# Performance work log

Measured on AMD Instinct MI355X. Metric: run time of the kernel, lower is better.

The kernel has to match this reference:

```python
import jax, jax.numpy as jnp
import numpy as np

BETA = 0.25

def _l2norm(x, eps=1e-12):
    # F.normalize(x, dim=-1)
    n = jnp.sqrt(jnp.sum(x * x, axis=-1, keepdims=True))
    return x / jnp.maximum(n, eps)

def setup_inputs() -> dict:
    key = jax.random.key(0)
    k1, k2 = jax.random.split(key)
    z = jax.random.normal(k1, (32, 1024, 32), dtype=jnp.float32)
    embedding = jax.random.normal(k2, (8192, 32), dtype=jnp.float32)
    return {"z": z, "embedding": embedding}

def reference(z, embedding):
    B, T, D = z.shape
    zf = _l2norm(z.reshape(-1, D))            # [N, D]
    en = _l2norm(embedding)                   # [n_e, D]
    # squared distances: ||z||^2 + ||e||^2 - 2 z.e  -> [N, n_e]
    d = (jnp.sum(zf * zf, axis=1, keepdims=True)
         + jnp.sum(en * en, axis=1)
         - 2.0 * jnp.einsum('nd,kd->nk', zf, en))
    idx = jnp.argmin(d, axis=1).reshape(B, T)            # [B, T]
    z_q = embedding[idx]                                  # [B, T, D] gather
    z_qnorm = _l2norm(z_q)
    z_norm = _l2norm(z)
    loss = (BETA * jnp.mean((jax.lax.stop_gradient(z_qnorm) - z_norm) ** 2)
            + jnp.mean((z_qnorm - jax.lax.stop_gradient(z_norm)) ** 2))
    # straight-through estimator
    z_q_out = z + jax.lax.stop_gradient(z_qnorm - z)
    return z_q_out, loss, idx
```

## Files before the change

### kernel.cpp

```cpp
#include <hip/hip_runtime.h>
#include <math.h>


#define D 32
#define KCODES 8192
#define MARGIN 2.5e-4f
#define EPS 1e-12f

typedef short bf16x8 __attribute__((ext_vector_type(8)));
typedef unsigned short u16x8 __attribute__((ext_vector_type(8)));
typedef float f32x4 __attribute__((ext_vector_type(4)));

static __device__ __forceinline__ unsigned short f2bf(float x) {
  unsigned u = __float_as_uint(x);
  return (unsigned short)((u + 0x7FFFu + ((u >> 16) & 1u)) >> 16);
}
static __device__ __forceinline__ float bf2f(unsigned short s) {
  return __uint_as_float(((unsigned)s) << 16);
}
static __device__ __forceinline__ void gload_lds16(const void* g, void* l) {
  __builtin_amdgcn_global_load_lds(
      (const __attribute__((address_space(1))) void*)g,
      (__attribute__((address_space(3))) void*)l, 16, 0, 0);
}


__global__ __launch_bounds__(256) void k_prep(const float* __restrict__ z,
                                              const float* __restrict__ emb,
                                              float* __restrict__ en,
                                              float* __restrict__ en_h,
                                              unsigned short* __restrict__ eswz,
                                              unsigned short* __restrict__ zswz_hi,
                                              unsigned short* __restrict__ zswz_lo,
                                              int* __restrict__ cnt,
                                              float* __restrict__ loss,
                                              unsigned long long* __restrict__ mp2,
                                              int N) {
  int v = blockIdx.x * 256 + threadIdx.x;
  if (v == 0) { *cnt = 0; *loss = 0.f; }
  if (v >= KCODES + N) return;
  if (v >= KCODES) mp2[v - KCODES] = 0ull;
  const float* src = (v < KCODES) ? (emb + (size_t)v * D) : (z + (size_t)(v - KCODES) * D);

  float x[D];
  const float4* p = reinterpret_cast<const float4*>(src);
#pragma unroll
  for (int j = 0; j < D / 4; ++j) {
    float4 q = p[j];
    x[4 * j + 0] = q.x; x[4 * j + 1] = q.y; x[4 * j + 2] = q.z; x[4 * j + 3] = q.w;
  }
  float ss = 0.f;
#pragma unroll
  for (int j = 0; j < D; ++j) ss = fmaf(x[j], x[j], ss);
  float n = fmaxf(sqrtf(ss), EPS);
#pragma unroll
  for (int j = 0; j < D; ++j) x[j] = x[j] / n;

  unsigned short hi[D], lo[D];
#pragma unroll
  for (int j = 0; j < D; ++j) {
    hi[j] = f2bf(x[j]);
    lo[j] = f2bf(x[j] - bf2f(hi[j]));
  }

  if (v < KCODES) {
    float4* o = reinterpret_cast<float4*>(en + (size_t)v * D);
    float s2 = 0.f;
#pragma unroll
    for (int j = 0; j < D / 4; ++j) {
      float4 q = {x[4 * j], x[4 * j + 1], x[4 * j + 2], x[4 * j + 3]};
      s2 = fmaf(q.x, q.x, fmaf(q.y, q.y, fmaf(q.z, q.z, fmaf(q.w, q.w, s2))));
      o[j] = q;
    }
    en_h[v] = 0.5f * s2;
    int tl = v >> 4, m = v & 15;
#pragma unroll
    for (int q = 0; q < 4; ++q) {
      u16x8 hv, lv;
#pragma unroll
      for (int j = 0; j < 8; ++j) { hv[j] = hi[8 * q + j]; lv[j] = lo[8 * q + j]; }
      *(u16x8*)(eswz + (size_t)tl * 1024 + (q * 16 + m) * 8) = hv;
      *(u16x8*)(eswz + (size_t)tl * 1024 + 512 + (q * 16 + m) * 8) = lv;
    }
  } else {
    int r = v - KCODES;
    int g = r >> 4, m = r & 15;
#pragma unroll
    for (int q = 0; q < 4; ++q) {
      u16x8 hv, lv;
#pragma unroll
      for (int j = 0; j < 8; ++j) { hv[j] = hi[8 * q + j]; lv[j] = lo[8 * q + j]; }
      *(u16x8*)(zswz_hi + (size_t)g * 512 + (q * 16 + m) * 8) = hv;
      *(u16x8*)(zswz_lo + (size_t)g * 512 + (q * 16 + m) * 8) = lv;
    }
  }
}

__global__ __launch_bounds__(256, 2) void k_argmin_mfma(
    const unsigned short* __restrict__ zswz_hi,
    const unsigned short* __restrict__ zswz_lo,
    const unsigned short* __restrict__ eswz,
    int* __restrict__ idx_ws, int* __restrict__ list, int* __restrict__ cnt) {
  __shared__ unsigned short lds_sh[2][16384];

  const int tid = threadIdx.x;
  const int wid = tid >> 6, lane = tid & 63;
  const int lane15 = lane & 15, quad = lane >> 4;
  const int g = blockIdx.x * 4 + wid;

  const bf16x8 zhi = *(const bf16x8*)(zswz_hi + (size_t)g * 512 + lane * 8);
  const bf16x8 zlo = *(const bf16x8*)(zswz_lo + (size_t)g * 512 + lane * 8);

  float s1[4], s2[4];
  int kb[4];
#pragma unroll
  for (int r = 0; r < 4; ++r) { s1[r] = -3.4e38f; s2[r] = -3.4e38f; kb[r] = 0; }
  const f32x4 zero4 = {0.f, 0.f, 0.f, 0.f};

  const float4* gall = reinterpret_cast<const float4*>(eswz);
#pragma unroll
  for (int i = 0; i < 8; ++i) {
    int off = i * 256 + tid;
    gload_lds16(gall + off, (char*)&lds_sh[0][0] + (size_t)off * 16);
  }

  for (int c = 0; c < 32; ++c) {
    __syncthreads();
    if (c + 1 < 32) {
      const float4* gn = gall + (size_t)(c + 1) * 2048;
      char* dst = (char*)&lds_sh[(c + 1) & 1][0];
#pragma unroll
      for (int i = 0; i < 8; ++i) {
        int off = i * 256 + tid;
        gload_lds16(gn + off, dst + (size_t)off * 16);
      }
    }
    const unsigned short* buf = &lds_sh[c & 1][0];
    int kcur = c * 256 + lane15;
#pragma unroll
    for (int t = 0; t < 16; ++t) {
      bf16x8 bhi = *(const bf16x8*)(buf + t * 1024 + lane * 8);
      bf16x8 blo = *(const bf16x8*)(buf + t * 1024 + 512 + lane * 8);
      f32x4 acc = __builtin_amdgcn_mfma_f32_16x16x32_bf16(zhi, bhi, zero4, 0, 0, 0);
      acc = __builtin_amdgcn_mfma_f32_16x16x32_bf16(zhi, blo, acc, 0, 0, 0);
      acc = __builtin_amdgcn_mfma_f32_16x16x32_bf16(zlo, bhi, acc, 0, 0, 0);
#pragma unroll
      for (int r = 0; r < 4; ++r) {
        float cv = acc[r];
        bool cond = cv > s1[r];
        kb[r] = cond ? kcur : kb[r];
        s2[r] = fmaxf(s2[r], fminf(cv, s1[r]));
        s1[r] = fmaxf(s1[r], cv);
      }
      kcur += 16;
    }
  }

  unsigned long long packed[4];
#pragma unroll
  for (int r = 0; r < 4; ++r) {
    unsigned o = __float_as_uint(s1[r]);
    o = (o & 0x80000000u) ? ~o : (o | 0x80000000u);
    packed[r] = ((unsigned long long)o << 32) | (unsigned)(8191 - kb[r]);
  }
#pragma unroll
  for (int m = 1; m <= 8; m <<= 1) {
#pragma unroll
    for (int r = 0; r < 4; ++r) {
      unsigned long long op = __shfl_xor(packed[r], m, 64);
      float os1 = __shfl_xor(s1[r], m, 64);
      float os2 = __shfl_xor(s2[r], m, 64);
      s2[r] = fmaxf(fmaxf(s2[r], os2), fminf(s1[r], os1));
      s1[r] = fmaxf(s1[r], os1);
      packed[r] = (op > packed[r]) ? op : packed[r];
    }
  }
  if (lane15 == 0) {
#pragma unroll
    for (int r = 0; r < 4; ++r) {
      int row = g * 16 + quad * 4 + r;
      if (s1[r] - s2[r] < MARGIN) {
        int pos = atomicAdd(cnt, 1);
        list[pos] = row;
        idx_ws[row] = -(pos + 1);
      } else {
        idx_ws[row] = 8191 - (int)(unsigned)(packed[r] & 0xFFFFFFFFull);
      }
    }
  }
}

__global__ __launch_bounds__(256) void k_cleanup(const float* __restrict__ z,
                                                 const float* __restrict__ en,
                                                 const float* __restrict__ en_h,
                                                 const int* __restrict__ list,
                                                 const int* __restrict__ cnt,
                                                 unsigned long long* __restrict__ mp2) {
  __shared__ unsigned long long wred[4];
  const int tid = threadIdx.x;
  const int lane = tid & 63, wid = tid >> 6;
  const int ntask = (*cnt) * 32;

  for (int j = blockIdx.x; j < ntask; j += gridDim.x) {
    int i = j >> 5, kc = j & 31;
    int row = list[i];
    const float* zr = z + (size_t)row * D;
    float v[D];
    float ss = 0.f;
#pragma unroll
    for (int d = 0; d < D; ++d) v[d] = zr[d];
#pragma unroll
    for (int d = 0; d < D; ++d) ss = fmaf(v[d], v[d], ss);
    float n = fmaxf(sqrtf(ss), EPS);
#pragma unroll
    for (int d = 0; d < D; ++d) v[d] = v[d] / n;

    int k = kc * 256 + tid;
    const float4* er = reinterpret_cast<const float4*>(en + (size_t)k * D);
    float a = -en_h[k];
#pragma unroll
    for (int jj = 0; jj < 8; ++jj) {
      float4 e = er[jj];
      a = fmaf(v[4 * jj + 0], e.x, a);
      a = fmaf(v[4 * jj + 1], e.y, a);
      a = fmaf(v[4 * jj + 2], e.z, a);
      a = fmaf(v[4 * jj + 3], e.w, a);
    }
    unsigned o = __float_as_uint(a);
    o = (o & 0x80000000u) ? ~o : (o | 0x80000000u);
    unsigned long long pk = ((unsigned long long)o << 32) | (unsigned)(8191 - k);
#pragma unroll
    for (int m = 32; m >= 1; m >>= 1) {
      unsigned long long op = __shfl_xor(pk, m, 64);
      pk = (op > pk) ? op : pk;
    }
    if (lane == 0) wred[wid] = pk;
    __syncthreads();
    if (tid == 0) {
      unsigned long long m01 = (wred[0] > wred[1]) ? wred[0] : wred[1];
      unsigned long long m23 = (wred[2] > wred[3]) ? wred[2] : wred[3];
      atomicMax(&mp2[i], (m01 > m23) ? m01 : m23);
    }
    __syncthreads();
  }
}

__global__ __launch_bounds__(256) void k_epi(const float* __restrict__ z,
                                             const float* __restrict__ en,
                                             const int* __restrict__ idx_ws,
                                             const unsigned long long* __restrict__ mp2,
                                             float* __restrict__ out_z,
                                             float* __restrict__ loss,
                                             float* __restrict__ out_idx,
                                             float scale) {
  int row = blockIdx.x * 256 + threadIdx.x;
  int kb = idx_ws[row];
  if (kb < 0) {
    unsigned long long m = mp2[-kb - 1];
    kb = 8191 - (int)(unsigned)(m & 0xFFFFFFFFull);
  }
  out_idx[row] = (float)kb;

  const float4* p = reinterpret_cast<const float4*>(z + (size_t)row * D);
  float4 q[D / 4];
#pragma unroll
  for (int j = 0; j < D / 4; ++j) q[j] = p[j];
  float ss = 0.f;
#pragma unroll
  for (int j = 0; j < D / 4; ++j)
    ss = fmaf(q[j].x, q[j].x, fmaf(q[j].y, q[j].y, fmaf(q[j].z, q[j].z, fmaf(q[j].w, q[j].w, ss))));
  float n = fmaxf(sqrtf(ss), EPS);

  const float4* ep = reinterpret_cast<const float4*>(en + (size_t)kb * D);
  float4* op = reinterpret_cast<float4*>(out_z + (size_t)row * D);
  float s = 0.f;
#pragma unroll
  for (int j = 0; j < D / 4; ++j) {
    float4 e = ep[j];
    float4 o;
    o.x = q[j].x + (e.x - q[j].x);
    o.y = q[j].y + (e.y - q[j].y);
    o.z = q[j].z + (e.z - q[j].z);
    o.w = q[j].w + (e.w - q[j].w);
    op[j] = o;
    float dx = e.x - q[j].x / n;  float dy = e.y - q[j].y / n;
    float dz = e.z - q[j].z / n;  float dw = e.w - q[j].w / n;
    s = fmaf(dx, dx, fmaf(dy, dy, fmaf(dz, dz, fmaf(dw, dw, s))));
  }

#pragma unroll
  for (int off = 32; off > 0; off >>= 1) s += __shfl_down(s, off, 64);
  __shared__ float wsum[4];
  int lane = threadIdx.x & 63, wid = threadIdx.x >> 6;
  if (lane == 0) wsum[wid] = s;
  __syncthreads();
  if (threadIdx.x == 0) {
    float tt = (wsum[0] + wsum[1]) + (wsum[2] + wsum[3]);
    atomicAdd(loss, tt * scale);
  }
}

extern "C" void kernel_launch(void* const* d_in, const int* in_sizes, int n_in,
                              void* d_out, int out_size, void* d_ws, size_t ws_size,
                              hipStream_t stream) {
  const float* z = (const float*)d_in[0];
  const float* emb = (const float*)d_in[1];
  const int N = in_sizes[0] / D;
  const int K = in_sizes[1] / D;

  float* out = (float*)d_out;
  float* out_z = out;
  float* loss = out + (size_t)N * D;
  float* out_idx = out + (size_t)N * D + 1;

  char* w = (char*)d_ws;
  float* en = (float*)w;                         w += (size_t)K * D * 4;
  float* en_h = (float*)w;                       w += (size_t)K * 4;
  unsigned short* eswz = (unsigned short*)w;     w += (size_t)K * D * 2 * 2;
  unsigned short* zswz_hi = (unsigned short*)w;  w += (size_t)N * D * 2;
  unsigned short* zswz_lo = (unsigned short*)w;  w += (size_t)N * D * 2;
  int* idx_ws = (int*)w;                         w += (size_t)N * 4;
  int* list = (int*)w;                           w += (size_t)N * 4;
  unsigned long long* mp2 = (unsigned long long*)w; w += (size_t)N * 8;
  int* cnt = (int*)w;

  k_prep<<<dim3((K + N) / 256), 256, 0, stream>>>(
      z, emb, en, en_h, eswz, zswz_hi, zswz_lo, cnt, loss, mp2, N);

  k_argmin_mfma<<<dim3(N / 64), 256, 0, stream>>>(
      zswz_hi, zswz_lo, eswz, idx_ws, list, cnt);

  k_cleanup<<<dim3(4096), 256, 0, stream>>>(z, en, en_h, list, cnt, mp2);

  k_epi<<<dim3(N / 256), 256, 0, stream>>>(
      z, en, idx_ws, mp2, out_z, loss, out_idx, 1.25f / (float)((size_t)N * D));
}
```

Baseline: 188.3 us.

## Fuse z normalization into argmin kernel and pack score with index

Moves the per-row z normalization and bf16 hi/lo split out of the prep kernel and into the argmin kernel, so the z staging buffers and their global round-trip go away. The top-2 tracking now packs a truncated positive score with a 9-bit tile index into one unsigned word, which makes the inner compare cheaper. The score is kept positive by seeding the accumulator with a constant offset. LDS B-fragment loads are software-prefetched one step ahead. The packing loses low mantissa bits, so the near-tie margin is widened, which may send more rows to the cleanup pass. The cleanup grid is halved and mp2 is now zeroed per list entry.

```diff
diff --git a/kernel.cpp b/kernel.cpp
--- a/kernel.cpp
+++ b/kernel.cpp
@@ -4,7 +4,7 @@
 
 #define D 32
 #define KCODES 8192
-#define MARGIN 2.5e-4f
+#define MARGIN_Q 5.0e-4f
 #define EPS 1e-12f
 
 typedef short bf16x8 __attribute__((ext_vector_type(8)));
@@ -25,25 +25,18 @@
 }
 
 
-__global__ __launch_bounds__(256) void k_prep(const float* __restrict__ z,
-                                              const float* __restrict__ emb,
+__global__ __launch_bounds__(256) void k_prep(const float* __restrict__ emb,
                                               float* __restrict__ en,
                                               float* __restrict__ en_h,
                                               unsigned short* __restrict__ eswz,
-                                              unsigned short* __restrict__ zswz_hi,
-                                              unsigned short* __restrict__ zswz_lo,
                                               int* __restrict__ cnt,
-                                              float* __restrict__ loss,
-                                              unsigned long long* __restrict__ mp2,
-                                              int N) {
+                                              float* __restrict__ loss) {
   int v = blockIdx.x * 256 + threadIdx.x;
   if (v == 0) { *cnt = 0; *loss = 0.f; }
-  if (v >= KCODES + N) return;
-  if (v >= KCODES) mp2[v - KCODES] = 0ull;
-  const float* src = (v < KCODES) ? (emb + (size_t)v * D) : (z + (size_t)(v - KCODES) * D);
+  if (v >= KCODES) return;
 
   float x[D];
-  const float4* p = reinterpret_cast<const float4*>(src);
+  const float4* p = reinterpret_cast<const float4*>(emb + (size_t)v * D);
 #pragma unroll
   for (int j = 0; j < D / 4; ++j) {
     float4 q = p[j];
@@ -56,51 +49,38 @@
 #pragma unroll
   for (int j = 0; j < D; ++j) x[j] = x[j] / n;
 
+  float4* o = reinterpret_cast<float4*>(en + (size_t)v * D);
+  float s2 = 0.f;
+#pragma unroll
+  for (int j = 0; j < D / 4; ++j) {
+    float4 q = {x[4 * j], x[4 * j + 1], x[4 * j + 2], x[4 * j + 3]};
+    s2 = fmaf(q.x, q.x, fmaf(q.y, q.y, fmaf(q.z, q.z, fmaf(q.w, q.w, s2))));
+    o[j] = q;
+  }
+  en_h[v] = 0.5f * s2;
+
   unsigned short hi[D], lo[D];
 #pragma unroll
   for (int j = 0; j < D; ++j) {
     hi[j] = f2bf(x[j]);
     lo[j] = f2bf(x[j] - bf2f(hi[j]));
   }
-
-  if (v < KCODES) {
-    float4* o = reinterpret_cast<float4*>(en + (size_t)v * D);
-    float s2 = 0.f;
-#pragma unroll
-    for (int j = 0; j < D / 4; ++j) {
-      float4 q = {x[4 * j], x[4 * j + 1], x[4 * j + 2], x[4 * j + 3]};
-      s2 = fmaf(q.x, q.x, fmaf(q.y, q.y, fmaf(q.z, q.z, fmaf(q.w, q.w, s2))));
-      o[j] = q;
-    }
-    en_h[v] = 0.5f * s2;
-    int tl = v >> 4, m = v & 15;
-#pragma unroll
-    for (int q = 0; q < 4; ++q) {
-      u16x8 hv, lv;
-#pragma unroll
-      for (int j = 0; j < 8; ++j) { hv[j] = hi[8 * q + j]; lv[j] = lo[8 * q + j]; }
-      *(u16x8*)(eswz + (size_t)tl * 1024 + (q * 16 + m) * 8) = hv;
-      *(u16x8*)(eswz + (size_t)tl * 1024 + 512 + (q * 16 + m) * 8) = lv;
-    }
-  } else {
-    int r = v - KCODES;
-    int g = r >> 4, m = r & 15;
-#pragma unroll
-    for (int q = 0; q < 4; ++q) {
-      u16x8 hv, lv;
-#pragma unroll
-      for (int j = 0; j < 8; ++j) { hv[j] = hi[8 * q + j]; lv[j] = lo[8 * q + j]; }
-      *(u16x8*)(zswz_hi + (size_t)g * 512 + (q * 16 + m) * 8) = hv;
-      *(u16x8*)(zswz_lo + (size_t)g * 512 + (q * 16 + m) * 8) = lv;
-    }
+  int tl = v >> 4, m = v & 15;
+#pragma unroll
+  for (int q = 0; q < 4; ++q) {
+    u16x8 hv, lv;
+#pragma unroll
+    for (int j = 0; j < 8; ++j) { hv[j] = hi[8 * q + j]; lv[j] = lo[8 * q + j]; }
+    *(u16x8*)(eswz + (size_t)tl * 1024 + (q * 16 + m) * 8) = hv;
+    *(u16x8*)(eswz + (size_t)tl * 1024 + 512 + (q * 16 + m) * 8) = lv;
   }
 }
 
 __global__ __launch_bounds__(256, 2) void k_argmin_mfma(
-    const unsigned short* __restrict__ zswz_hi,
-    const unsigned short* __restrict__ zswz_lo,
+    const float* __restrict__ z,
     const unsigned short* __restrict__ eswz,
-    int* __restrict__ idx_ws, int* __restrict__ list, int* __restrict__ cnt) {
+    int* __restrict__ idx_ws, int* __restrict__ list, int* __restrict__ cnt,
+    unsigned long long* __restrict__ mp2) {
   __shared__ unsigned short lds_sh[2][16384];
 
   const int tid = threadIdx.x;
@@ -108,21 +88,39 @@
   const int lane15 = lane & 15, quad = lane >> 4;
   const int g = blockIdx.x * 4 + wid;
 
-  const bf16x8 zhi = *(const bf16x8*)(zswz_hi + (size_t)g * 512 + lane * 8);
-  const bf16x8 zlo = *(const bf16x8*)(zswz_lo + (size_t)g * 512 + lane * 8);
-
-  float s1[4], s2[4];
-  int kb[4];
-#pragma unroll
-  for (int r = 0; r < 4; ++r) { s1[r] = -3.4e38f; s2[r] = -3.4e38f; kb[r] = 0; }
-  const f32x4 zero4 = {0.f, 0.f, 0.f, 0.f};
-
   const float4* gall = reinterpret_cast<const float4*>(eswz);
 #pragma unroll
   for (int i = 0; i < 8; ++i) {
     int off = i * 256 + tid;
     gload_lds16(gall + off, (char*)&lds_sh[0][0] + (size_t)off * 16);
   }
+
+  bf16x8 zhi, zlo;
+  {
+    const float4* p = reinterpret_cast<const float4*>(z + (size_t)(g * 16 + lane15) * D);
+    float ss = 0.f;
+#pragma unroll
+    for (int j = 0; j < 8; ++j) {
+      float4 q = p[j];
+      ss = fmaf(q.x, q.x, fmaf(q.y, q.y, fmaf(q.z, q.z, fmaf(q.w, q.w, ss))));
+    }
+    float nn = fmaxf(sqrtf(ss), EPS);
+    float4 a0 = p[quad * 2], a1 = p[quad * 2 + 1];
+    float xs[8] = {a0.x / nn, a0.y / nn, a0.z / nn, a0.w / nn,
+                   a1.x / nn, a1.y / nn, a1.z / nn, a1.w / nn};
+#pragma unroll
+    for (int j = 0; j < 8; ++j) {
+      unsigned short h = f2bf(xs[j]);
+      zhi[j] = (short)h;
+      zlo[j] = (short)f2bf(xs[j] - bf2f(h));
+    }
+  }
+
+  unsigned p1[4], p2[4];
+#pragma unroll
+  for (int r = 0; r < 4; ++r) { p1[r] = 0u; p2[r] = 0u; }
+  const f32x4 initA = {1.25f, 1.25f, 1.25f, 1.25f};
+  const f32x4 zero4 = {0.f, 0.f, 0.f, 0.f};
 
   for (int c = 0; c < 32; ++c) {
     __syncthreads();
@@ -136,55 +134,58 @@
       }
     }
     const unsigned short* buf = &lds_sh[c & 1][0];
-    int kcur = c * 256 + lane15;
+    bf16x8 cbh = *(const bf16x8*)(buf + lane * 8);
+    bf16x8 cbl = *(const bf16x8*)(buf + 512 + lane * 8);
+    const unsigned tbase = (unsigned)(511 - c * 16);
 #pragma unroll
     for (int t = 0; t < 16; ++t) {
-      bf16x8 bhi = *(const bf16x8*)(buf + t * 1024 + lane * 8);
-      bf16x8 blo = *(const bf16x8*)(buf + t * 1024 + 512 + lane * 8);
-      f32x4 acc = __builtin_amdgcn_mfma_f32_16x16x32_bf16(zhi, bhi, zero4, 0, 0, 0);
-      acc = __builtin_amdgcn_mfma_f32_16x16x32_bf16(zhi, blo, acc, 0, 0, 0);
-      acc = __builtin_amdgcn_mfma_f32_16x16x32_bf16(zlo, bhi, acc, 0, 0, 0);
+      bf16x8 nbh, nbl;
+      if (t < 15) {
+        nbh = *(const bf16x8*)(buf + (t + 1) * 1024 + lane * 8);
+        nbl = *(const bf16x8*)(buf + (t + 1) * 1024 + 512 + lane * 8);
+      }
+      f32x4 aa = __builtin_amdgcn_mfma_f32_16x16x32_bf16(zhi, cbh, initA, 0, 0, 0);
+      f32x4 ab = __builtin_amdgcn_mfma_f32_16x16x32_bf16(zhi, cbl, zero4, 0, 0, 0);
+      ab = __builtin_amdgcn_mfma_f32_16x16x32_bf16(zlo, cbh, ab, 0, 0, 0);
+      const unsigned tid9 = tbase - t;
 #pragma unroll
       for (int r = 0; r < 4; ++r) {
-        float cv = acc[r];
-        bool cond = cv > s1[r];
-        kb[r] = cond ? kcur : kb[r];
-        s2[r] = fmaxf(s2[r], fminf(cv, s1[r]));
-        s1[r] = fmaxf(s1[r], cv);
+        float sa = aa[r] + ab[r];
+        unsigned pk = (__float_as_uint(sa) & 0xFFFFFE00u) | tid9;
+        unsigned tmin = (pk < p1[r]) ? pk : p1[r];
+        p1[r] = (pk > p1[r]) ? pk : p1[r];
+        p2[r] = (tmin > p2[r]) ? tmin : p2[r];
       }
-      kcur += 16;
-    }
-  }
-
-  unsigned long long packed[4];
+      cbh = nbh; cbl = nbl;
+    }
+  }
+
 #pragma unroll
   for (int r = 0; r < 4; ++r) {
-    unsigned o = __float_as_uint(s1[r]);
-    o = (o & 0x80000000u) ? ~o : (o | 0x80000000u);
-    packed[r] = ((unsigned long long)o << 32) | (unsigned)(8191 - kb[r]);
-  }
-#pragma unroll
-  for (int m = 1; m <= 8; m <<= 1) {
-#pragma unroll
-    for (int r = 0; r < 4; ++r) {
-      unsigned long long op = __shfl_xor(packed[r], m, 64);
-      float os1 = __shfl_xor(s1[r], m, 64);
-      float os2 = __shfl_xor(s2[r], m, 64);
-      s2[r] = fmaxf(fmaxf(s2[r], os2), fminf(s1[r], os1));
-      s1[r] = fmaxf(s1[r], os1);
-      packed[r] = (op > packed[r]) ? op : packed[r];
-    }
-  }
-  if (lane15 == 0) {
-#pragma unroll
-    for (int r = 0; r < 4; ++r) {
-      int row = g * 16 + quad * 4 + r;
-      if (s1[r] - s2[r] < MARGIN) {
+    int kl = (511 - (int)(p1[r] & 511u)) * 16 + lane15;
+    unsigned sb = p1[r] & 0xFFFFFE00u;
+    float s1f = __uint_as_float(sb);
+    float s2f = __uint_as_float(p2[r] & 0xFFFFFE00u);
+    unsigned long long pk =
+        ((unsigned long long)sb << 32) | (unsigned)(8191 - kl);
+#pragma unroll
+    for (int m = 1; m <= 8; m <<= 1) {
+      unsigned long long op = __shfl_xor(pk, m, 64);
+      float os1 = __shfl_xor(s1f, m, 64);
+      float os2 = __shfl_xor(s2f, m, 64);
+      s2f = fmaxf(fmaxf(s2f, os2), fminf(s1f, os1));
+      s1f = fmaxf(s1f, os1);
+      pk = (op > pk) ? op : pk;
+    }
+    if (lane15 == 0) {
+      int orow = g * 16 + quad * 4 + r;
+      if (s1f - s2f < MARGIN_Q) {
         int pos = atomicAdd(cnt, 1);
-        list[pos] = row;
-        idx_ws[row] = -(pos + 1);
+        list[pos] = orow;
+        mp2[pos] = 0ull;
+        idx_ws[orow] = -(pos + 1);
       } else {
-        idx_ws[row] = 8191 - (int)(unsigned)(packed[r] & 0xFFFFFFFFull);
+        idx_ws[orow] = 8191 - (int)(unsigned)(pk & 0xFFFFFFFFull);
       }
     }
   }
@@ -317,20 +318,17 @@
   float* en = (float*)w;                         w += (size_t)K * D * 4;
   float* en_h = (float*)w;                       w += (size_t)K * 4;
   unsigned short* eswz = (unsigned short*)w;     w += (size_t)K * D * 2 * 2;
-  unsigned short* zswz_hi = (unsigned short*)w;  w += (size_t)N * D * 2;
-  unsigned short* zswz_lo = (unsigned short*)w;  w += (size_t)N * D * 2;
   int* idx_ws = (int*)w;                         w += (size_t)N * 4;
   int* list = (int*)w;                           w += (size_t)N * 4;
   unsigned long long* mp2 = (unsigned long long*)w; w += (size_t)N * 8;
   int* cnt = (int*)w;
 
-  k_prep<<<dim3((K + N) / 256), 256, 0, stream>>>(
-      z, emb, en, en_h, eswz, zswz_hi, zswz_lo, cnt, loss, mp2, N);
+  k_prep<<<dim3(K / 256), 256, 0, stream>>>(emb, en, en_h, eswz, cnt, loss);
 
   k_argmin_mfma<<<dim3(N / 64), 256, 0, stream>>>(
-      zswz_hi, zswz_lo, eswz, idx_ws, list, cnt);
-
-  k_cleanup<<<dim3(4096), 256, 0, stream>>>(z, en, en_h, list, cnt, mp2);
+      z, eswz, idx_ws, list, cnt, mp2);
+
+  k_cleanup<<<dim3(2048), 256, 0, stream>>>(z, en, en_h, list, cnt, mp2);
 
   k_epi<<<dim3(N / 256), 256, 0, stream>>>(
       z, en, idx_ws, mp2, out_z, loss, out_idx, 1.25f / (float)((size_t)N * D));
```

Result: slower. 210.0 us (+11.5%).
